# Optimization experiments

Measured on AMD Instinct MI355X. Metric: run time of the kernel, lower is better.

The kernel has to match this reference:

```python
import jax, jax.numpy as jnp
import numpy as np
from jax import lax

KS = 3            # kernel_size
K = 32            # cluster_num
NB = 32           # num_base_kernels
HID = 64          # mlp_hidden_dim
COUT = 64         # out_channels
MAX_ITER = 20
TOL = 0.005


def _unfold3(x):
    # torch nn.Unfold(k=3, pad=1): output channel order is (c, kh, kw)
    b, c, h, w = x.shape
    xp = jnp.pad(x, ((0, 0), (0, 0), (1, 1), (1, 1)))
    cols = [xp[:, :, i:i + h, j:j + w] for i in range(KS) for j in range(KS)]
    p = jnp.stack(cols, axis=2)  # [B, C, 9, H, W]
    return p.reshape(b, c * KS * KS, h * w).transpose(0, 2, 1)  # [B, HW, C*9]


def _kmeans_single(key, sample):
    # sample: [N, D]. Lloyd iterations with early stop on total center shift.
    n, d = sample.shape
    centers0 = sample[jax.random.permutation(key, n)[:K]]

    def assign(centers):
        d2 = (jnp.sum(sample * sample, 1, keepdims=True)
              - 2.0 * (sample @ centers.T)
              + jnp.sum(centers * centers, 1))
        return jnp.argmin(d2, axis=1)

    def body(carry):
        i, centers, _ = carry
        a = assign(centers)
        oh = jax.nn.one_hot(a, K, dtype=sample.dtype)  # [N, K]
        counts = oh.sum(0)                             # [K]
        sums = oh.T @ sample                           # [K, D]
        new = jnp.where(counts[:, None] > 0,
                        sums / jnp.maximum(counts, 1.0)[:, None],
                        centers)
        shift = jnp.sum(jnp.linalg.norm(new - centers, axis=1))
        return (i + 1, new, shift)

    def cond(carry):
        i, _, shift = carry
        return jnp.logical_and(i < MAX_ITER, shift >= TOL * n)

    init = (jnp.int32(0), centers0, jnp.asarray(jnp.inf, sample.dtype))
    _, centers, _ = lax.while_loop(cond, body, init)
    return assign(centers)


def _kmeans(features):
    keys = jax.random.split(jax.random.key(42), features.shape[0])
    return jax.vmap(_kmeans_single)(keys, features)


def _mlp(x, w1, b1, w2, b2, w3, b3):
    h = jax.nn.relu(x @ w1 + b1)
    h = jax.nn.relu(h @ w2 + b2)
    return h @ w3 + b3


def setup_inputs() -> dict:
    key = jax.random.key(0)
    ks = jax.random.split(key, 16)
    B, C, H, W = 2, 32, 64, 64
    F = C * KS * KS
    fan = 1.0 / np.sqrt(F)
    fanh = 1.0 / np.sqrt(HID)
    return {
        'x': jax.random.normal(ks[0], (B, C, H, W), jnp.float32),
        'base_kernels': jax.random.normal(ks[1], (NB, F, COUT), jnp.float32) * np.sqrt(2.0 / F),
        'kg_w1': jax.random.normal(ks[2], (F, HID), jnp.float32) * fan,
        'kg_b1': jnp.zeros((HID,), jnp.float32),
        'kg_w2': jax.random.normal(ks[3], (HID, HID), jnp.float32) * fanh,
        'kg_b2': jnp.zeros((HID,), jnp.float32),
        'kg_w3': jax.random.normal(ks[4], (HID, NB), jnp.float32) * fanh,
        'kg_b3': jnp.zeros((NB,), jnp.float32),
        'bg_w1': jax.random.normal(ks[5], (F, HID), jnp.float32) * fan,
        'bg_b1': jnp.zeros((HID,), jnp.float32),
        'bg_w2': jax.random.normal(ks[6], (HID, HID), jnp.float32) * fanh,
        'bg_b2': jnp.zeros((HID,), jnp.float32),
        'bg_w3': jax.random.normal(ks[7], (HID, COUT), jnp.float32) * fanh,
        'bg_b3': jnp.zeros((COUT,), jnp.float32),
    }


def reference(x, base_kernels, kg_w1, kg_b1, kg_w2, kg_b2, kg_w3, kg_b3,
              bg_w1, bg_b1, bg_w2, bg_b2, bg_w3, bg_b3):
    B, C, H, W = x.shape
    patches = _unfold3(x)  # [B, P, F] with F = C*9
    P = patches.shape[1]
    # observation features: mean over kernel area per channel
    obs = patches.reshape(B, P, C, KS * KS).mean(-1)  # [B, P, C]
    idx = _kmeans(obs)  # [B, P] int cluster assignments

    # per-cluster centers of the full patch features (scatter-mean)
    oh = jax.nn.one_hot(idx, K, dtype=patches.dtype)          # [B, P, K]
    sums = jnp.einsum('bpk,bpf->bkf', oh, patches)            # [B, K, F]
    counts = jnp.maximum(oh.sum(1), 1.0)                      # [B, K]
    centers = sums / counts[:, :, None]                       # [B, K, F]

    # adaptive kernels = softmax-mixture of base kernels
    attn = jax.nn.softmax(_mlp(centers, kg_w1, kg_b1, kg_w2, kg_b2, kg_w3, kg_b3), axis=-1)  # [B,K,NB]
    kernels = jnp.einsum('bkn,nfc->bkfc', attn, base_kernels)  # [B, K, F, COUT]
    biases = _mlp(centers, bg_w1, bg_b1, bg_w2, bg_b2, bg_w3, bg_b3)  # [B, K, COUT]

    # combine: out[b,p] = patches[b,p] @ kernels[b, idx[b,p]] + biases[b, idx[b,p]]
    bidx = jnp.arange(B)[:, None]
    wtok = kernels[bidx, idx]   # [B, P, F, COUT]
    btok = biases[bidx, idx]    # [B, P, COUT]
    out = jnp.einsum('bpf,bpfc->bpc', patches, wtok) + btok
    out = out.transpose(0, 2, 1).reshape(B, COUT, H, W)
    return (out, idx)
```

## Files before the change

### kernel.cpp

```cpp
#include <hip/hip_runtime.h>
#include <hip/hip_bf16.h>
#include <vector>
#include <algorithm>
#include <utility>
#include <stdint.h>

#define BB 2
#define PP 4096
#define FF 288
#define KK 32
#define NBASE 32
#define HID 64
#define COUT 64
#define NWG_KM 32
#define SUBS 16
#define OUT_ELEMS 524288

#define THREEFRY_PARTITIONABLE 1

typedef unsigned short u16;

#define OFF_IDX    512
#define OFF_BIAS   41472
#define OFF_PART   57856
#define OFF_CNTS   320000
#define OFF_CPART  328192
#define OFF_WG     1544704
#define OFF_BAR2   3904000

struct InitIdx { int v[2][32]; };

__device__ __forceinline__ float bf2f(u16 u){
  union { unsigned int i; float f; } cv; cv.i = ((unsigned int)u) << 16; return cv.f;
}
__device__ __forceinline__ u16 f2bf(float f){
  union { float f; unsigned int i; } cv; cv.f = f;
  unsigned int x = cv.i;
  unsigned int r = (x + 0x7FFFu + ((x >> 16) & 1u)) >> 16;
  return (u16)r;
}
__device__ __forceinline__ float u_lo(unsigned int u){
  union { unsigned int i; float f; } cv; cv.i = u << 16; return cv.f;
}
__device__ __forceinline__ float u_hi(unsigned int u){
  union { unsigned int i; float f; } cv; cv.i = u & 0xFFFF0000u; return cv.f;
}

__device__ __forceinline__ void st_agent(float* p, float v){
  __hip_atomic_store(reinterpret_cast<unsigned int*>(p), __float_as_uint(v),
                     __ATOMIC_RELAXED, __HIP_MEMORY_SCOPE_AGENT);
}
__device__ __forceinline__ float ld_agent(const float* p){
  unsigned int u = __hip_atomic_load(reinterpret_cast<const unsigned int*>(p),
                                     __ATOMIC_RELAXED, __HIP_MEMORY_SCOPE_AGENT);
  return __uint_as_float(u);
}
__device__ __forceinline__ void st_slot(int* p, int v){
  __hip_atomic_store(p, v, __ATOMIC_RELAXED, __HIP_MEMORY_SCOPE_AGENT);
}
__device__ __forceinline__ int ld_slot(const int* p){
  return __hip_atomic_load(p, __ATOMIC_RELAXED, __HIP_MEMORY_SCOPE_AGENT);
}

template<bool BF>
__device__ __forceinline__ float ld(const void* p, size_t i){
  if constexpr (BF) { return bf2f(((const u16*)p)[i]); }
  else              { return ((const float*)p)[i]; }
}
template<bool BF>
__device__ __forceinline__ void st(void* p, size_t i, float v){
  if constexpr (BF) { ((u16*)p)[i] = f2bf(v); }
  else              { ((float*)p)[i] = v; }
}

__device__ __forceinline__ bool self_detect(const void* x, int* cntS){
  const int t = threadIdx.x, nb = blockDim.x;
  if (t == 0) *cntS = 0;
  __syncthreads();
  const u16* p = (const u16*)x;
  int bad = 0;
  for (int i = t; i < 1024; i += nb){
    u16 u = p[2*i];
    unsigned e = (u >> 7) & 0xFFu;
    if (e >= 131u) ++bad;
  }
  if (bad) atomicAdd(cntS, bad);
  __syncthreads();
  bool r = (*cntS < 102);
  __syncthreads();
  return r;
}

template<bool BF>
__device__ __forceinline__ float obs_chan(const void* x, size_t bi, int h, int w){
  float s = 0.f;
  #pragma unroll
  for (int dh=-1; dh<=1; ++dh){
    int hh = h + dh;
    #pragma unroll
    for (int dw=-1; dw<=1; ++dw){
      int ww = w + dw;
      float v = 0.f;
      if ((unsigned)hh < 64u && (unsigned)ww < 64u) v = ld<BF>(x, bi + (hh<<6) + ww);
      s += v;
    }
  }
  return s / 9.0f;
}

__device__ __forceinline__ void gbar16(int* slots, int mb, int sub, int epoch){
  asm volatile("s_waitcnt vmcnt(0)" ::: "memory");
  __syncthreads();
  const int t = threadIdx.x;
  if (t == 0) st_slot(&slots[(mb*16 + sub)*16], epoch);
  if (t < 16){
    while (ld_slot(&slots[(mb*16 + t)*16]) < epoch){}
  }
  __atomic_signal_fence(__ATOMIC_SEQ_CST);
  __syncthreads();
}

template<bool BF>
__device__ void kB_body(const void* __restrict__ x,
                        float* __restrict__ part,
                        float* __restrict__ cnts,
                        int* __restrict__ idxg,
                        void* __restrict__ dout,
                        int* __restrict__ slots,
                        const InitIdx& ii,
                        float* obs_st, float* cent, float* cc_s, int* a_loc,
                        float* sq, float* snorm, float* cntsh,
                        float* acc8, float* cnt8){
  const int t   = threadIdx.x;
  const int wg  = blockIdx.x;
  const int mb  = wg >> 4;
  const int sub = wg & 15;
  const int pg  = sub*256 + t;
  const int d   = t & 31, oct = t >> 5;

  float o[32];
  {
    int h = pg >> 6, w = pg & 63;
    size_t xb = (size_t)mb << 17;
    for (int c=0; c<32; ++c){
      float v = obs_chan<BF>(x, xb + ((size_t)c<<12), h, w);
      o[c] = v; obs_st[t*33 + c] = v;
    }
  }
  if (t < 32){
    int q = ii.v[mb][t];
    int qh = q >> 6, qw = q & 63;
    size_t xq = (size_t)mb << 17;
    for (int c=0; c<32; ++c) cent[t*32 + c] = obs_chan<BF>(x, xq + ((size_t)c<<12), qh, qw);
  }
  __syncthreads();

  float ss = 0.f;
  #pragma unroll
  for (int dd=0; dd<32; ++dd) ss = fmaf(o[dd], o[dd], ss);

  bool act = true;
  int parity = 0;

  for (int it=0; it<20 && act; ++it){
    if (t < 32){
      float s = 0.f;
      #pragma unroll
      for (int dd=0; dd<32; ++dd){ float v = cent[t*32 + dd]; s = fmaf(v,v,s); }
      cc_s[t] = s;
    }
    __syncthreads();
    float best = 3.0e38f; int bk = 0;
    for (int k=0; k<32; k+=4){
      const float4* c0 = (const float4*)&cent[(k  )*32];
      const float4* c1 = (const float4*)&cent[(k+1)*32];
      const float4* c2 = (const float4*)&cent[(k+2)*32];
      const float4* c3 = (const float4*)&cent[(k+3)*32];
      float dt0=0.f, dt1=0.f, dt2=0.f, dt3=0.f;
      #pragma unroll
      for (int q=0; q<8; ++q){
        float4 a0 = c0[q], a1 = c1[q], a2 = c2[q], a3 = c3[q];
        float o0 = o[q*4+0], o1 = o[q*4+1], o2 = o[q*4+2], o3 = o[q*4+3];
        dt0 = fmaf(o0,a0.x,dt0); dt0 = fmaf(o1,a0.y,dt0); dt0 = fmaf(o2,a0.z,dt0); dt0 = fmaf(o3,a0.w,dt0);
        dt1 = fmaf(o0,a1.x,dt1); dt1 = fmaf(o1,a1.y,dt1); dt1 = fmaf(o2,a1.z,dt1); dt1 = fmaf(o3,a1.w,dt1);
        dt2 = fmaf(o0,a2.x,dt2); dt2 = fmaf(o1,a2.y,dt2); dt2 = fmaf(o2,a2.z,dt2); dt2 = fmaf(o3,a2.w,dt2);
        dt3 = fmaf(o0,a3.x,dt3); dt3 = fmaf(o1,a3.y,dt3); dt3 = fmaf(o2,a3.z,dt3); dt3 = fmaf(o3,a3.w,dt3);
      }
      float di0 = (ss - 2.0f*dt0) + cc_s[k];
      float di1 = (ss - 2.0f*dt1) + cc_s[k+1];
      float di2 = (ss - 2.0f*dt2) + cc_s[k+2];
      float di3 = (ss - 2.0f*dt3) + cc_s[k+3];
      if (di0 < best){ best = di0; bk = k; }
      if (di1 < best){ best = di1; bk = k+1; }
      if (di2 < best){ best = di2; bk = k+2; }
      if (di3 < best){ best = di3; bk = k+3; }
    }
    a_loc[t] = bk;
    __syncthreads();
    for (int e=t; e<8*32*33; e+=256) acc8[e] = 0.f;
    cnt8[t] = 0.f;
    __syncthreads();
    {
      const int p0 = oct*32;
      int kcur = a_loc[p0];
      float racc = 0.f; int rl = 0;
      for (int i=0; i<32; ++i){
        int kp = a_loc[p0+i];
        float v = obs_st[(p0+i)*33 + d];
        if (kp != kcur){
          acc8[(oct*32 + kcur)*33 + d] += racc;
          if (d == 0) cnt8[oct*32 + kcur] += (float)rl;
          racc = 0.f; rl = 0; kcur = kp;
        }
        racc += v; ++rl;
      }
      acc8[(oct*32 + kcur)*33 + d] += racc;
      if (d == 0) cnt8[oct*32 + kcur] += (float)rl;
    }
    __syncthreads();
    float* Pg = part + ((size_t)((parity*2 + mb)*SUBS + sub))*1024;
    {
      float r0=0.f, r1=0.f, r2=0.f, r3=0.f;
      #pragma unroll
      for (int o2=0; o2<8; ++o2){
        r0 += acc8[(o2*32 + oct      )*33 + d];
        r1 += acc8[(o2*32 + oct + 8  )*33 + d];
        r2 += acc8[(o2*32 + oct + 16 )*33 + d];
        r3 += acc8[(o2*32 + oct + 24 )*33 + d];
      }
      st_agent(&Pg[(oct     )*32 + d], r0);
      st_agent(&Pg[(oct + 8 )*32 + d], r1);
      st_agent(&Pg[(oct + 16)*32 + d], r2);
      st_agent(&Pg[(oct + 24)*32 + d], r3);
    }
    if (t < 32){
      float c = 0.f;
      #pragma unroll
      for (int o2=0; o2<8; ++o2) c += cnt8[o2*32 + t];
      st_agent(&cnts[((size_t)((parity*2 + mb)*SUBS + sub))*32 + t], c);
    }
    gbar16(slots, mb, sub, it+1);
    {
      const float* Pb = part + (size_t)((parity*2 + mb)*SUBS)*1024;
      const float* Cb = cnts + (size_t)((parity*2 + mb)*SUBS)*32;
      if (t < 32){
        float s = 0.f;
        #pragma unroll
        for (int si=0; si<SUBS; ++si) s += ld_agent(&Cb[si*32 + t]);
        cntsh[t] = s;
      }
      __syncthreads();
      {
        int k = t >> 3, d4 = (t & 7) * 4;
        float vx = 0.f, vy = 0.f, vz = 0.f, vw = 0.f;
        #pragma unroll
        for (int si=0; si<SUBS; ++si){
          const float* pp = &Pb[si*1024 + k*32 + d4];
          float a0 = ld_agent(pp+0);
          float a1 = ld_agent(pp+1);
          float a2 = ld_agent(pp+2);
          float a3 = ld_agent(pp+3);
          vx += a0; vy += a1; vz += a2; vw += a3;
        }
        float cn = cntsh[k];
        float den = fmaxf(cn, 1.f);
        bool pos = cn > 0.f;
        float o0 = cent[k*32 + d4+0], o1 = cent[k*32 + d4+1];
        float o2 = cent[k*32 + d4+2], o3 = cent[k*32 + d4+3];
        float n0 = pos ? (vx / den) : o0;
        float n1 = pos ? (vy / den) : o1;
        float n2 = pos ? (vz / den) : o2;
        float n3 = pos ? (vw / den) : o3;
        float e0 = n0-o0, e1 = n1-o1, e2 = n2-o2, e3 = n3-o3;
        sq[k*32 + d4+0] = e0*e0; sq[k*32 + d4+1] = e1*e1;
        sq[k*32 + d4+2] = e2*e2; sq[k*32 + d4+3] = e3*e3;
        cent[k*32 + d4+0] = n0; cent[k*32 + d4+1] = n1;
        cent[k*32 + d4+2] = n2; cent[k*32 + d4+3] = n3;
      }
      __syncthreads();
      if (t < 32){
        float s = 0.f;
        #pragma unroll
        for (int dd=0; dd<32; ++dd) s += sq[t*32 + dd];
        snorm[t] = sqrtf(s);
      }
      __syncthreads();
      float sh = 0.f;
      for (int k=0;k<32;++k) sh += snorm[k];
      act = ((it+1) < 20) && ((double)sh >= 20.48);
      __syncthreads();
    }
    parity ^= 1;
  }
  if (t == 0) st_slot(&slots[(mb*16 + sub)*16], 0x7FFFFFFF);
  __syncthreads();
  if (t < 32){
    float s = 0.f;
    #pragma unroll
    for (int dd=0; dd<32; ++dd){ float v = cent[t*32 + dd]; s = fmaf(v,v,s); }
    cc_s[t] = s;
  }
  __syncthreads();
  float best = 3.0e38f; int bk = 0;
  for (int k=0; k<32; k+=4){
    const float4* c0 = (const float4*)&cent[(k  )*32];
    const float4* c1 = (const float4*)&cent[(k+1)*32];
    const float4* c2 = (const float4*)&cent[(k+2)*32];
    const float4* c3 = (const float4*)&cent[(k+3)*32];
    float dt0=0.f, dt1=0.f, dt2=0.f, dt3=0.f;
    #pragma unroll
    for (int q=0; q<8; ++q){
      float4 a0 = c0[q], a1 = c1[q], a2 = c2[q], a3 = c3[q];
      float o0 = o[q*4+0], o1 = o[q*4+1], o2 = o[q*4+2], o3 = o[q*4+3];
      dt0 = fmaf(o0,a0.x,dt0); dt0 = fmaf(o1,a0.y,dt0); dt0 = fmaf(o2,a0.z,dt0); dt0 = fmaf(o3,a0.w,dt0);
      dt1 = fmaf(o0,a1.x,dt1); dt1 = fmaf(o1,a1.y,dt1); dt1 = fmaf(o2,a1.z,dt1); dt1 = fmaf(o3,a1.w,dt1);
      dt2 = fmaf(o0,a2.x,dt2); dt2 = fmaf(o1,a2.y,dt2); dt2 = fmaf(o2,a2.z,dt2); dt2 = fmaf(o3,a2.w,dt2);
      dt3 = fmaf(o0,a3.x,dt3); dt3 = fmaf(o1,a3.y,dt3); dt3 = fmaf(o2,a3.z,dt3); dt3 = fmaf(o3,a3.w,dt3);
    }
    float di0 = (ss - 2.0f*dt0) + cc_s[k];
    float di1 = (ss - 2.0f*dt1) + cc_s[k+1];
    float di2 = (ss - 2.0f*dt2) + cc_s[k+2];
    float di3 = (ss - 2.0f*dt3) + cc_s[k+3];
    if (di0 < best){ best = di0; bk = k; }
    if (di1 < best){ best = di1; bk = k+1; }
    if (di2 < best){ best = di2; bk = k+2; }
    if (di3 < best){ best = di3; bk = k+3; }
  }
  idxg[mb*PP + pg] = bk;
  st<BF>(dout, (size_t)OUT_ELEMS + mb*PP + pg, (float)bk);
}

__global__ __launch_bounds__(256) void kB(const void* x, float* part, float* cnts,
                                          int* idxg, void* dout,
                                          int* slots, InitIdx ii){
  __shared__ __align__(16) float obs_st[256*33];
  __shared__ __align__(16) float cent[32*32];
  __shared__ float cc_s[32];
  __shared__ int   a_loc[256];
  __shared__ float sq[32*32];
  __shared__ float snorm[32];
  __shared__ float cntsh[32];
  __shared__ float acc8[8*32*33];
  __shared__ float cnt8[8*32];
  __shared__ int   cntS;
  if (self_detect(x, &cntS))
       kB_body<true >(x, part, cnts, idxg, dout, slots, ii,
                      obs_st, cent, cc_s, a_loc, sq, snorm, cntsh, acc8, cnt8);
  else kB_body<false>(x, part, cnts, idxg, dout, slots, ii,
                      obs_st, cent, cc_s, a_loc, sq, snorm, cntsh, acc8, cnt8);
}

template<bool BF>
__device__ void kC_body(const void* __restrict__ x,
                        const int* __restrict__ idxg,
                        float* __restrict__ cpartJ,
                        float* __restrict__ tv,
                        int* __restrict__ idxsh,
                        float* __restrict__ acc8,
                        float* __restrict__ cnt8){
  int wgid = blockIdx.x;
  int cg = wgid / 9, j = wgid % 9;
  int b = cg >> 4, pc = cg & 15;
  int t = threadIdx.x;
  const int d = t & 31, oct = t >> 5;

  idxsh[t] = idxg[b*PP + pc*256 + t];
  int dh = j/3 - 1, dw = j%3 - 1;
  for (int e=t; e<8192; e+=256){
    int c = e >> 8, p = e & 255;
    int gp = (pc << 8) + p;
    int h = gp >> 6, w = gp & 63;
    int hh = h + dh, ww = w + dw;
    float v = 0.f;
    if ((unsigned)hh < 64u && (unsigned)ww < 64u)
      v = ld<BF>(x, ((size_t)b << 17) + ((size_t)c << 12) + (hh<<6) + ww);
    tv[p*33 + c] = v;
  }
  for (int e=t; e<8*32*33; e+=256) acc8[e] = 0.f;
  cnt8[t] = 0.f;
  __syncthreads();
  {
    const int p0 = oct*32;
    int kcur = idxsh[p0];
    float racc = 0.f; int rl = 0;
    for (int i=0; i<32; ++i){
      int kp = idxsh[p0+i];
      float v = tv[(p0+i)*33 + d];
      if (kp != kcur){
        acc8[(oct*32 + kcur)*33 + d] += racc;
        if (d == 0) cnt8[oct*32 + kcur] += (float)rl;
        racc = 0.f; rl = 0; kcur = kp;
      }
      racc += v; ++rl;
    }
    acc8[(oct*32 + kcur)*33 + d] += racc;
    if (d == 0) cnt8[oct*32 + kcur] += (float)rl;
  }
  __syncthreads();
  float* cp = cpartJ + (size_t)wgid*(32*33);
  {
    float r0=0.f, r1=0.f, r2=0.f, r3=0.f;
    #pragma unroll
    for (int o2=0; o2<8; ++o2){
      r0 += acc8[(o2*32 + oct      )*33 + d];
      r1 += acc8[(o2*32 + oct + 8  )*33 + d];
      r2 += acc8[(o2*32 + oct + 16 )*33 + d];
      r3 += acc8[(o2*32 + oct + 24 )*33 + d];
    }
    cp[(oct     )*33 + d] = r0;
    cp[(oct + 8 )*33 + d] = r1;
    cp[(oct + 16)*33 + d] = r2;
    cp[(oct + 24)*33 + d] = r3;
  }
  if (j == 0 && t < 32){
    float c8 = 0.f;
    #pragma unroll
    for (int o2=0; o2<8; ++o2) c8 += cnt8[o2*32 + t];
    cp[t*33 + 32] = c8;
  }
}

__global__ __launch_bounds__(256) void kC(const void* x, const int* idxg,
                                          float* cpartJ){
  __shared__ __align__(16) float tv[256*33];
  __shared__ int   idxsh[256];
  __shared__ __align__(16) float acc8[8*32*33];
  __shared__ float cnt8[256];
  __shared__ int   cntS;
  if (self_detect(x, &cntS)) kC_body<true >(x, idxg, cpartJ, tv, idxsh, acc8, cnt8);
  else                       kC_body<false>(x, idxg, cpartJ, tv, idxsh, acc8, cnt8);
}

template<bool BF>
__device__ void kDE_body(const void* __restrict__ base,
                         const float* __restrict__ cpartJ,
                         const void* kg_w1, const void* kg_b1,
                         const void* kg_w2, const void* kg_b2,
                         const void* kg_w3, const void* kg_b3,
                         const void* bg_w1, const void* bg_b1,
                         const void* bg_w2, const void* bg_b2,
                         const void* bg_w3, const void* bg_b3,
                         float* __restrict__ biasO,
                         u16* __restrict__ Wg,
                         float* row, float* h1, float* h2, float* lgs,
                         float* at, float* tile){
  int wg = blockIdx.x;
  int fq = wg & 3, bk = wg >> 2;
  int b = bk >> 5, k = bk & 31;
  int t = threadIdx.x;

  if (t < 64){
    float cnt = 0.f;
    for (int ch=0; ch<16; ++ch)
      cnt += cpartJ[(size_t)((b*16+ch)*9)*(32*33) + k*33 + 32];
    float den = fmaxf(cnt, 1.f);
    for (int f=t; f<FF; f+=64){
      int c = f / 9, j = f % 9;
      float s = 0.f;
      for (int ch=0; ch<16; ++ch)
        s += cpartJ[(size_t)((b*16+ch)*9 + j)*(32*33) + k*33 + c];
      row[f] = s / den;
    }
  }
  __syncthreads();
  if (t < 64){
    float s = 0.f;
    #pragma unroll 8
    for (int f=0; f<FF; ++f) s = fmaf(row[f], ld<BF>(kg_w1, f*HID + t), s);
    h1[t] = fmaxf(s + ld<BF>(kg_b1, t), 0.f);
  }
  __syncthreads();
  if (t < 64){
    float s = 0.f;
    #pragma unroll 8
    for (int h=0; h<HID; ++h) s = fmaf(h1[h], ld<BF>(kg_w2, h*HID + t), s);
    h2[t] = fmaxf(s + ld<BF>(kg_b2, t), 0.f);
  }
  __syncthreads();
  if (t < 32){
    float s = 0.f;
    #pragma unroll 8
    for (int h=0; h<HID; ++h) s = fmaf(h2[h], ld<BF>(kg_w3, h*NBASE + t), s);
    lgs[t] = s + ld<BF>(kg_b3, t);
  }
  __syncthreads();
  if (t < 32){
    float mx = -3.0e38f;
    for (int i=0;i<NBASE;++i) mx = fmaxf(mx, lgs[i]);
    float se = 0.f;
    for (int i=0;i<NBASE;++i) se += expf(lgs[i]-mx);
    at[t] = expf(lgs[t]-mx) / se;
  }
  __syncthreads();
  if (t < 64){
    float s = 0.f;
    #pragma unroll 8
    for (int f=0; f<FF; ++f) s = fmaf(row[f], ld<BF>(bg_w1, f*HID + t), s);
    h1[t] = fmaxf(s + ld<BF>(bg_b1, t), 0.f);
  }
  __syncthreads();
  if (t < 64){
    float s = 0.f;
    #pragma unroll 8
    for (int h=0; h<HID; ++h) s = fmaf(h1[h], ld<BF>(bg_w2, h*HID + t), s);
    h2[t] = fmaxf(s + ld<BF>(bg_b2, t), 0.f);
  }
  __syncthreads();
  if (t < 64 && fq == 0){
    float s = 0.f;
    #pragma unroll 8
    for (int h=0; h<HID; ++h) s = fmaf(h2[h], ld<BF>(bg_w3, h*COUT + t), s);
    biasO[bk*COUT + t] = s + ld<BF>(bg_b3, t);
  }
  __syncthreads();

  int f0 = fq*72;
  for (int e8 = t; e8 < 72*8; e8 += 256){
    int fl = e8 >> 3, cg = (e8 & 7) << 3;
    float s0=0.f,s1=0.f,s2=0.f,s3=0.f,s4=0.f,s5=0.f,s6=0.f,s7=0.f;
    if constexpr (BF){
      const u16* bp = (const u16*)base + (size_t)(f0 + fl)*COUT + cg;
      #pragma unroll 4
      for (int n=0; n<NBASE; ++n){
        uint4 v = *(const uint4*)(bp + (size_t)n*FF*COUT);
        float a = at[n];
        s0 = fmaf(a, u_lo(v.x), s0); s1 = fmaf(a, u_hi(v.x), s1);
        s2 = fmaf(a, u_lo(v.y), s2); s3 = fmaf(a, u_hi(v.y), s3);
        s4 = fmaf(a, u_lo(v.z), s4); s5 = fmaf(a, u_hi(v.z), s5);
        s6 = fmaf(a, u_lo(v.w), s6); s7 = fmaf(a, u_hi(v.w), s7);
      }
    } else {
      const float* bp = (const float*)base + (size_t)(f0 + fl)*COUT + cg;
      #pragma unroll 4
      for (int n=0; n<NBASE; ++n){
        float4 v0 = *(const float4*)(bp + (size_t)n*FF*COUT);
        float4 v1 = *(const float4*)(bp + (size_t)n*FF*COUT + 4);
        float a = at[n];
        s0 = fmaf(a, v0.x, s0); s1 = fmaf(a, v0.y, s1);
        s2 = fmaf(a, v0.z, s2); s3 = fmaf(a, v0.w, s3);
        s4 = fmaf(a, v1.x, s4); s5 = fmaf(a, v1.y, s5);
        s6 = fmaf(a, v1.z, s6); s7 = fmaf(a, v1.w, s7);
      }
    }
    float* tp = &tile[fl*65 + cg];
    tp[0]=s0; tp[1]=s1; tp[2]=s2; tp[3]=s3;
    tp[4]=s4; tp[5]=s5; tp[6]=s6; tp[7]=s7;
  }
  __syncthreads();
  for (int e=t; e<72*64; e+=256){
    int c = e / 72, fl = e % 72;
    Wg[(size_t)bk*(64*FF) + (size_t)c*FF + f0 + fl] = f2bf(tile[fl*65 + c]);
  }
}

__global__ __launch_bounds__(256) void kDE(const void* x, const void* base,
                         const float* cpartJ,
                         const void* kg_w1, const void* kg_b1,
                         const void* kg_w2, const void* kg_b2,
                         const void* kg_w3, const void* kg_b3,
                         const void* bg_w1, const void* bg_b1,
                         const void* bg_w2, const void* bg_b2,
                         const void* bg_w3, const void* bg_b3,
                         float* biasO, u16* Wg){
  __shared__ float row[FF];
  __shared__ float h1[64];
  __shared__ float h2[64];
  __shared__ float lgs[32];
  __shared__ float at[32];
  __shared__ float tile[72*65];
  __shared__ int   cntS;
  if (self_detect(x, &cntS))
       kDE_body<true >(base, cpartJ, kg_w1,kg_b1,kg_w2,kg_b2,kg_w3,kg_b3,
                       bg_w1,bg_b1,bg_w2,bg_b2,bg_w3,bg_b3, biasO, Wg,
                       row,h1,h2,lgs,at,tile);
  else kDE_body<false>(base, cpartJ, kg_w1,kg_b1,kg_w2,kg_b2,kg_w3,kg_b3,
                       bg_w1,bg_b1,bg_w2,bg_b2,bg_w3,bg_b3, biasO, Wg,
                       row,h1,h2,lgs,at,tile);
}

template<bool BF>
__device__ void kF_body(const void* __restrict__ x,
                        const int* __restrict__ idxg,
                        const u16* __restrict__ Wg,
                        const float* __restrict__ biasO,
                        void* __restrict__ dout,
                        u16* __restrict__ patch,
                        float* __restrict__ outT){
  int wg = blockIdx.x;
  int q = wg & 3, h = (wg >> 2) & 63, b = wg >> 8;
  int t = threadIdx.x, wv = t >> 6, lane = t & 63;
  int w0 = q << 4;

  for (int e=t; e<16*FF; e+=256){
    int pl = e & 15, fe = e >> 4;
    int c = fe / 9, j = fe % 9;
    int hh = h + j/3 - 1, ww = w0 + pl + (j%3) - 1;
    float v = 0.f;
    if ((unsigned)hh < 64u && (unsigned)ww < 64u)
      v = ld<BF>(x, ((size_t)b << 17) + ((size_t)c << 12) + (hh<<6) + ww);
    patch[pl*296 + fe] = f2bf(v);
  }
  __syncthreads();

  #pragma unroll
  for (int i=0; i<4; ++i){
    int pl = (wv << 2) + i;
    int p = (h << 6) + w0 + pl;
    int k = idxg[(b << 12) + p];
    const uint4* Wp = (const uint4*)(Wg + ((size_t)((b << 5) + k)*64 + lane)*FF);
    const uint4* Pp = (const uint4*)(patch + pl*296);
    float acc = 0.f;
    #pragma unroll 6
    for (int j=0; j<36; ++j){
      uint4 wv4 = Wp[j];
      uint4 pv4 = Pp[j];
      acc = fmaf(u_lo(pv4.x), u_lo(wv4.x), acc);
      acc = fmaf(u_hi(pv4.x), u_hi(wv4.x), acc);
      acc = fmaf(u_lo(pv4.y), u_lo(wv4.y), acc);
      acc = fmaf(u_hi(pv4.y), u_hi(wv4.y), acc);
      acc = fmaf(u_lo(pv4.z), u_lo(wv4.z), acc);
      acc = fmaf(u_hi(pv4.z), u_hi(wv4.z), acc);
      acc = fmaf(u_lo(pv4.w), u_lo(wv4.w), acc);
      acc = fmaf(u_hi(pv4.w), u_hi(wv4.w), acc);
    }
    float bias = biasO[((b << 5) + k)*COUT + lane];
    outT[lane*17 + pl] = acc + bias;
  }
  __syncthreads();

  for (int e=t; e<1024; e+=256){
    int cout = e >> 4, pl = e & 15;
    st<BF>(dout, (((size_t)(b << 6) + cout) << 12) + (h << 6) + w0 + pl,
           outT[cout*17 + pl]);
  }
}

__global__ __launch_bounds__(256) void kF(const void* x, const int* idxg,
                                          const u16* Wg, const float* biasO,
                                          void* dout){
  __shared__ u16   patch[16*296];
  __shared__ float outT[64*17];
  __shared__ int   cntS;
  if (self_detect(x, &cntS)) kF_body<true >(x, idxg, Wg, biasO, dout, patch, outT);
  else                       kF_body<false>(x, idxg, Wg, biasO, dout, patch, outT);
}

static inline uint32_t rotl32(uint32_t x, int d){ return (x<<d)|(x>>(32-d)); }
static void tf_block(uint32_t k0,uint32_t k1,uint32_t x0,uint32_t x1,uint32_t&o0,uint32_t&o1){
  uint32_t ks2 = k0 ^ k1 ^ 0x1BD11BDAu;
  uint32_t v0 = x0 + k0, v1 = x1 + k1;
  const int ra[4]={13,15,26,6}, rb[4]={17,29,16,24};
  #define R4(r) for(int i_=0;i_<4;++i_){ v0 += v1; v1 = rotl32(v1,(r)[i_]); v1 ^= v0; }
  R4(ra); v0 += k1;  v1 += ks2 + 1u;
  R4(rb); v0 += ks2; v1 += k0  + 2u;
  R4(ra); v0 += k0;  v1 += k1  + 3u;
  R4(rb); v0 += k1;  v1 += ks2 + 4u;
  R4(ra); v0 += ks2; v1 += k0  + 5u;
  #undef R4
  o0 = v0; o1 = v1;
}
struct KP{ uint32_t a, b; };
static void tf_split(KP k, KP& first, KP& second){
#if THREEFRY_PARTITIONABLE
  uint32_t a0,b0,a1,b1;
  tf_block(k.a,k.b, 0u,0u, a0,b0);
  tf_block(k.a,k.b, 0u,1u, a1,b1);
  first  = KP{a0,b0};
  second = KP{a1,b1};
#else
  uint32_t a0,b0,a1,b1;
  tf_block(k.a,k.b, 0u,2u, a0,b0);
  tf_block(k.a,k.b, 1u,3u, a1,b1);
  first  = KP{a0,a1};
  second = KP{b0,b1};
#endif
}
static void random_bits_4096(KP k, std::vector<uint32_t>& bits){
#if THREEFRY_PARTITIONABLE
  for (int i=0;i<4096;++i){
    uint32_t o0,o1; tf_block(k.a,k.b, 0u,(uint32_t)i, o0,o1);
    bits[i] = o0 ^ o1;
  }
#else
  for (int i=0;i<2048;++i){
    uint32_t o0,o1; tf_block(k.a,k.b,(uint32_t)i,(uint32_t)(i+2048),o0,o1);
    bits[i] = o0; bits[i+2048] = o1;
  }
#endif
}
static void perm_first32(KP key, int* out32){
  std::vector<int> vals(4096);
  for (int i=0;i<4096;++i) vals[i] = i;
  std::vector<uint32_t> bits(4096);
  std::vector<std::pair<uint32_t,int>> pr(4096);
  KP k = key;
  for (int r=0;r<2;++r){
    KP nk, sk; tf_split(k, nk, sk); k = nk;
    random_bits_4096(sk, bits);
    for (int i=0;i<4096;++i) pr[i] = std::make_pair(bits[i], vals[i]);
    std::stable_sort(pr.begin(), pr.end(),
        [](const std::pair<uint32_t,int>& a, const std::pair<uint32_t,int>& c){ return a.first < c.first; });
    for (int i=0;i<4096;++i) vals[i] = pr[i].second;
  }
  for (int j=0;j<32;++j) out32[j] = vals[j];
}

static const InitIdx& get_init_idx(){
  static const InitIdx ii = [](){
    InitIdx r;
    KP root = KP{0u, 42u};
    KP kb0, kb1; tf_split(root, kb0, kb1);
    perm_first32(kb0, r.v[0]);
    perm_first32(kb1, r.v[1]);
    return r;
  }();
  return ii;
}

extern "C" void kernel_launch(void* const* d_in, const int* in_sizes, int n_in,
                              void* d_out, int out_size, void* d_ws, size_t ws_size,
                              hipStream_t stream) {
  const void* x     = d_in[0];
  const void* base  = d_in[1];
  const void* kg_w1 = d_in[2];
  const void* kg_b1 = d_in[3];
  const void* kg_w2 = d_in[4];
  const void* kg_b2 = d_in[5];
  const void* kg_w3 = d_in[6];
  const void* kg_b3 = d_in[7];
  const void* bg_w1 = d_in[8];
  const void* bg_b1 = d_in[9];
  const void* bg_w2 = d_in[10];
  const void* bg_b2 = d_in[11];
  const void* bg_w3 = d_in[12];
  const void* bg_b3 = d_in[13];

  char* ws = (char*)d_ws;
  int*   idxg  = (int*)(ws + OFF_IDX);
  float* biasO = (float*)(ws + OFF_BIAS);
  float* part  = (float*)(ws + OFF_PART);
  float* cnts  = (float*)(ws + OFF_CNTS);
  float* cpartJ= (float*)(ws + OFF_CPART);
  u16*   Wg    = (u16*)(ws + OFF_WG);
  int*   slots = (int*)(ws + OFF_BAR2);

  const InitIdx& ii = get_init_idx();

  hipMemsetAsync(ws + OFF_BAR2, 0, 2048, stream);
  kB<<<NWG_KM, 256, 0, stream>>>(x, part, cnts, idxg, d_out, slots, ii);
  kC<<<288, 256, 0, stream>>>(x, idxg, cpartJ);
  kDE<<<256, 256, 0, stream>>>(x, base, cpartJ,
                               kg_w1, kg_b1, kg_w2, kg_b2, kg_w3, kg_b3,
                               bg_w1, bg_b1, bg_w2, bg_b2, bg_w3, bg_b3,
                               biasO, Wg);
  kF<<<512, 256, 0, stream>>>(x, idxg, Wg, biasO, d_out);
}
```

Before: 265.5 us.

## Fuse scatter-mean, kernel-gen and apply stages into one persistent kernel with flags

```diff
diff --git a/kernel.cpp b/kernel.cpp
--- a/kernel.cpp
+++ b/kernel.cpp
@@ -54,6 +54,9 @@
   unsigned int u = __hip_atomic_load(reinterpret_cast<const unsigned int*>(p),
                                      __ATOMIC_RELAXED, __HIP_MEMORY_SCOPE_AGENT);
   return __uint_as_float(u);
+}
+__device__ __forceinline__ void st_agent_u32(unsigned int* p, unsigned int v){
+  __hip_atomic_store(p, v, __ATOMIC_RELAXED, __HIP_MEMORY_SCOPE_AGENT);
 }
 __device__ __forceinline__ void st_slot(int* p, int v){
   __hip_atomic_store(p, v, __ATOMIC_RELAXED, __HIP_MEMORY_SCOPE_AGENT);
@@ -351,14 +354,13 @@
 }
 
 template<bool BF>
-__device__ void kC_body(const void* __restrict__ x,
+__device__ void kC_item(int wgid, const void* __restrict__ x,
                         const int* __restrict__ idxg,
                         float* __restrict__ cpartJ,
                         float* __restrict__ tv,
                         int* __restrict__ idxsh,
                         float* __restrict__ acc8,
                         float* __restrict__ cnt8){
-  int wgid = blockIdx.x;
   int cg = wgid / 9, j = wgid % 9;
   int b = cg >> 4, pc = cg & 15;
   int t = threadIdx.x;
@@ -407,32 +409,21 @@
       r2 += acc8[(o2*32 + oct + 16 )*33 + d];
       r3 += acc8[(o2*32 + oct + 24 )*33 + d];
     }
-    cp[(oct     )*33 + d] = r0;
-    cp[(oct + 8 )*33 + d] = r1;
-    cp[(oct + 16)*33 + d] = r2;
-    cp[(oct + 24)*33 + d] = r3;
+    st_agent(&cp[(oct     )*33 + d], r0);
+    st_agent(&cp[(oct + 8 )*33 + d], r1);
+    st_agent(&cp[(oct + 16)*33 + d], r2);
+    st_agent(&cp[(oct + 24)*33 + d], r3);
   }
   if (j == 0 && t < 32){
     float c8 = 0.f;
     #pragma unroll
     for (int o2=0; o2<8; ++o2) c8 += cnt8[o2*32 + t];
-    cp[t*33 + 32] = c8;
-  }
-}
-
-__global__ __launch_bounds__(256) void kC(const void* x, const int* idxg,
-                                          float* cpartJ){
-  __shared__ __align__(16) float tv[256*33];
-  __shared__ int   idxsh[256];
-  __shared__ __align__(16) float acc8[8*32*33];
-  __shared__ float cnt8[256];
-  __shared__ int   cntS;
-  if (self_detect(x, &cntS)) kC_body<true >(x, idxg, cpartJ, tv, idxsh, acc8, cnt8);
-  else                       kC_body<false>(x, idxg, cpartJ, tv, idxsh, acc8, cnt8);
+    st_agent(&cp[t*33 + 32], c8);
+  }
 }
 
 template<bool BF>
-__device__ void kDE_body(const void* __restrict__ base,
+__device__ void kDE_item(int wg, const void* __restrict__ base,
                          const float* __restrict__ cpartJ,
                          const void* kg_w1, const void* kg_b1,
                          const void* kg_w2, const void* kg_b2,
@@ -444,7 +435,6 @@
                          u16* __restrict__ Wg,
                          float* row, float* h1, float* h2, float* lgs,
                          float* at, float* tile){
-  int wg = blockIdx.x;
   int fq = wg & 3, bk = wg >> 2;
   int b = bk >> 5, k = bk & 31;
   int t = threadIdx.x;
@@ -510,7 +500,7 @@
     float s = 0.f;
     #pragma unroll 8
     for (int h=0; h<HID; ++h) s = fmaf(h2[h], ld<BF>(bg_w3, h*COUT + t), s);
-    biasO[bk*COUT + t] = s + ld<BF>(bg_b3, t);
+    st_agent(&biasO[bk*COUT + t], s + ld<BF>(bg_b3, t));
   }
   __syncthreads();
 
@@ -547,49 +537,33 @@
     tp[4]=s4; tp[5]=s5; tp[6]=s6; tp[7]=s7;
   }
   __syncthreads();
-  for (int e=t; e<72*64; e+=256){
-    int c = e / 72, fl = e % 72;
-    Wg[(size_t)bk*(64*FF) + (size_t)c*FF + f0 + fl] = f2bf(tile[fl*65 + c]);
-  }
-}
-
-__global__ __launch_bounds__(256) void kDE(const void* x, const void* base,
-                         const float* cpartJ,
-                         const void* kg_w1, const void* kg_b1,
-                         const void* kg_w2, const void* kg_b2,
-                         const void* kg_w3, const void* kg_b3,
-                         const void* bg_w1, const void* bg_b1,
-                         const void* bg_w2, const void* bg_b2,
-                         const void* bg_w3, const void* bg_b3,
-                         float* biasO, u16* Wg){
-  __shared__ float row[FF];
-  __shared__ float h1[64];
-  __shared__ float h2[64];
-  __shared__ float lgs[32];
-  __shared__ float at[32];
-  __shared__ float tile[72*65];
-  __shared__ int   cntS;
-  if (self_detect(x, &cntS))
-       kDE_body<true >(base, cpartJ, kg_w1,kg_b1,kg_w2,kg_b2,kg_w3,kg_b3,
-                       bg_w1,bg_b1,bg_w2,bg_b2,bg_w3,bg_b3, biasO, Wg,
-                       row,h1,h2,lgs,at,tile);
-  else kDE_body<false>(base, cpartJ, kg_w1,kg_b1,kg_w2,kg_b2,kg_w3,kg_b3,
-                       bg_w1,bg_b1,bg_w2,bg_b2,bg_w3,bg_b3, biasO, Wg,
-                       row,h1,h2,lgs,at,tile);
+  for (int e=t; e<72*32; e+=256){
+    int c = e / 36, fp = (e % 36) * 2;
+    unsigned lo = f2bf(tile[(fp  )*65 + c]);
+    unsigned hi = f2bf(tile[(fp+1)*65 + c]);
+    unsigned* wp = (unsigned*)(Wg + (size_t)bk*(64*FF) + (size_t)c*FF + f0 + fp);
+    st_agent_u32(wp, lo | (hi << 16));
+  }
 }
 
 template<bool BF>
-__device__ void kF_body(const void* __restrict__ x,
+__device__ void kF_item(int item, const void* __restrict__ x,
                         const int* __restrict__ idxg,
                         const u16* __restrict__ Wg,
                         const float* __restrict__ biasO,
                         void* __restrict__ dout,
+                        const int* __restrict__ wgflag,
                         u16* __restrict__ patch,
                         float* __restrict__ outT){
-  int wg = blockIdx.x;
-  int q = wg & 3, h = (wg >> 2) & 63, b = wg >> 8;
+  int q = item & 3, h = (item >> 2) & 63, b = item >> 8;
   int t = threadIdx.x, wv = t >> 6, lane = t & 63;
   int w0 = q << 4;
+
+  if (t < 16){
+    int kk = idxg[(b << 12) + (h << 6) + w0 + t];
+    while (ld_slot(&wgflag[(b << 5) + kk]) < 4) __builtin_amdgcn_s_sleep(8);
+  }
+  __syncthreads();
 
   for (int e=t; e<16*FF; e+=256){
     int pl = e & 15, fe = e >> 4;
@@ -635,14 +609,69 @@
   }
 }
 
-__global__ __launch_bounds__(256) void kF(const void* x, const int* idxg,
-                                          const u16* Wg, const float* biasO,
-                                          void* dout){
-  __shared__ u16   patch[16*296];
-  __shared__ float outT[64*17];
-  __shared__ int   cntS;
-  if (self_detect(x, &cntS)) kF_body<true >(x, idxg, Wg, biasO, dout, patch, outT);
-  else                       kF_body<false>(x, idxg, Wg, biasO, dout, patch, outT);
+template<bool BF>
+__device__ void kCDEF_body(const void* x, const void* base,
+                           const int* idxg, float* cpartJ,
+                           const void* kg_w1, const void* kg_b1,
+                           const void* kg_w2, const void* kg_b2,
+                           const void* kg_w3, const void* kg_b3,
+                           const void* bg_w1, const void* bg_b1,
+                           const void* bg_w2, const void* bg_b2,
+                           const void* bg_w3, const void* bg_b3,
+                           float* biasO, u16* Wg, void* dout,
+                           int* flags, char* sm){
+  const int wg = blockIdx.x, t = threadIdx.x;
+  int* cntC   = flags;
+  int* wgflag = flags + 16;
+
+  if (wg < 288){
+    kC_item<BF>(wg, x, idxg, cpartJ,
+                (float*)(sm + 0), (int*)(sm + 67584),
+                (float*)(sm + 33792), (float*)(sm + 68608));
+    asm volatile("s_waitcnt vmcnt(0)" ::: "memory");
+    __syncthreads();
+    if (t == 0) atomicAdd(cntC, 1);
+  }
+
+  if (wg < 256){
+    if (t == 0){
+      while (ld_slot(cntC) < 288) __builtin_amdgcn_s_sleep(8);
+    }
+    __syncthreads();
+    kDE_item<BF>(wg, base, cpartJ, kg_w1,kg_b1,kg_w2,kg_b2,kg_w3,kg_b3,
+                 bg_w1,bg_b1,bg_w2,bg_b2,bg_w3,bg_b3, biasO, Wg,
+                 (float*)(sm + 0), (float*)(sm + 1152), (float*)(sm + 1408),
+                 (float*)(sm + 1664), (float*)(sm + 1792), (float*)(sm + 1920));
+    asm volatile("s_waitcnt vmcnt(0)" ::: "memory");
+    __syncthreads();
+    if (t == 0) atomicAdd(&wgflag[wg >> 2], 1);
+  }
+  __syncthreads();
+
+  kF_item<BF>(wg, x, idxg, Wg, biasO, dout, wgflag,
+              (u16*)(sm + 0), (float*)(sm + 9472));
+}
+
+__global__ __launch_bounds__(256) void kCDEF(const void* x, const void* base,
+                           const int* idxg, float* cpartJ,
+                           const void* kg_w1, const void* kg_b1,
+                           const void* kg_w2, const void* kg_b2,
+                           const void* kg_w3, const void* kg_b3,
+                           const void* bg_w1, const void* bg_b1,
+                           const void* bg_w2, const void* bg_b2,
+                           const void* bg_w3, const void* bg_b3,
+                           float* biasO, u16* Wg, void* dout, int* flags){
+  __shared__ __align__(16) char sm[69632];
+  __shared__ int cntS;
+  if (self_detect(x, &cntS))
+       kCDEF_body<true >(x, base, idxg, cpartJ,
+                         kg_w1,kg_b1,kg_w2,kg_b2,kg_w3,kg_b3,
+                         bg_w1,bg_b1,bg_w2,bg_b2,bg_w3,bg_b3,
+                         biasO, Wg, dout, flags, sm);
+  else kCDEF_body<false>(x, base, idxg, cpartJ,
+                         kg_w1,kg_b1,kg_w2,kg_b2,kg_w3,kg_b3,
+                         bg_w1,bg_b1,bg_w2,bg_b2,bg_w3,bg_b3,
+                         biasO, Wg, dout, flags, sm);
 }
 
 static inline uint32_t rotl32(uint32_t x, int d){ return (x<<d)|(x>>(32-d)); }
@@ -743,15 +772,14 @@
   float* cpartJ= (float*)(ws + OFF_CPART);
   u16*   Wg    = (u16*)(ws + OFF_WG);
   int*   slots = (int*)(ws + OFF_BAR2);
+  int*   flags = (int*)(ws + OFF_BAR2 + 2048);
 
   const InitIdx& ii = get_init_idx();
 
-  hipMemsetAsync(ws + OFF_BAR2, 0, 2048, stream);
+  hipMemsetAsync(ws + OFF_BAR2, 0, 3072, stream);
   kB<<<NWG_KM, 256, 0, stream>>>(x, part, cnts, idxg, d_out, slots, ii);
-  kC<<<288, 256, 0, stream>>>(x, idxg, cpartJ);
-  kDE<<<256, 256, 0, stream>>>(x, base, cpartJ,
-                               kg_w1, kg_b1, kg_w2, kg_b2, kg_w3, kg_b3,
-                               bg_w1, bg_b1, bg_w2, bg_b2, bg_w3, bg_b3,
-                               biasO, Wg);
-  kF<<<512, 256, 0, stream>>>(x, idxg, Wg, biasO, d_out);
-}
+  kCDEF<<<512, 256, 0, stream>>>(x, base, idxg, cpartJ,
+                                 kg_w1, kg_b1, kg_w2, kg_b2, kg_w3, kg_b3,
+                                 bg_w1, bg_b1, bg_w2, bg_b2, bg_w3, bg_b3,
+                                 biasO, Wg, d_out, flags);
+}
```

Result: slower. 274.0 us (+3.2%).
